# Kernel optimization log

Hardware: AMD Instinct MI355X
Metric: run time of the kernel (lower is better)

The kernel has to match this reference:

```python
import jax, jax.numpy as jnp
import numpy as np

D_MODEL = 1024
NHEAD = 16
HEAD_DIM = D_MODEL // NHEAD
SCALE = HEAD_DIM ** (-0.5)


def setup_inputs() -> dict:
    key = jax.random.key(0)
    k1, k2, k3 = jax.random.split(key, 3)
    B, T, C = 2, 2048, D_MODEL
    x = jax.random.normal(k1, (B, T, C), dtype=jnp.float32)
    W_qkv = jax.random.normal(k2, (3 * C, C), dtype=jnp.float32) * (C ** -0.5)
    b_qkv = jnp.zeros((3 * C,), dtype=jnp.float32)
    W_out = jax.random.normal(k3, (C, C), dtype=jnp.float32) * (C ** -0.5)
    b_out = jnp.zeros((C,), dtype=jnp.float32)
    return {"x": x, "W_qkv": W_qkv, "b_qkv": b_qkv, "W_out": W_out, "b_out": b_out}


def reference(x, W_qkv, b_qkv, W_out, b_out):
    B, T, C = x.shape
    H, hd = NHEAD, HEAD_DIM
    qkv = x @ W_qkv.T + b_qkv
    qkv = qkv.reshape(B, T, 3, H, hd).transpose(2, 0, 3, 1, 4)
    q, k, v = qkv[0], qkv[1], qkv[2]
    # scaled dot-product scores: (B,H,T,T)
    attn = jnp.einsum('bhqd,bhkd->bhqk', q, k) * SCALE
    # causal mask (is_causal=True): lower-triangular allowed
    causal = jnp.tril(jnp.ones((T, T), dtype=bool))
    attn = jnp.where(causal[None, None, :, :], attn, -jnp.inf)
    attn = jax.nn.softmax(attn, axis=-1)
    # (B,H,T,hd) -> (B,T,C)
    out = jnp.einsum('bhqk,bhkd->bhqd', attn, v)
    out = out.transpose(0, 2, 1, 3).reshape(B, T, C)
    out = out @ W_out.T + b_out
    return out
```

## Files before the change

kernel.cpp:

```cpp
#include <hip/hip_runtime.h>
#include <hip/hip_bf16.h>
#include <stdint.h>

#define D_MODEL 1024
#define NHEAD   16
#define HEAD_DIM 64
#define BATCH   2
#define SEQ     2048
#define M_TOK   (BATCH*SEQ)
#define N_QKV   (3*D_MODEL)
#define KDIM    1024
#define Q_SCALE (0.125f * 1.44269504088896f)

typedef __bf16 bf16_t;
typedef bf16_t bf16x8 __attribute__((ext_vector_type(8)));
typedef bf16_t bf16x4 __attribute__((ext_vector_type(4)));
typedef float  f32x4  __attribute__((ext_vector_type(4)));

__device__ __forceinline__ void gl_lds16(const void* g, void* l) {
    __builtin_amdgcn_global_load_lds(
        (__attribute__((address_space(1))) void*)(void*)(const_cast<void*>(g)),
        (__attribute__((address_space(3))) void*)l, 16, 0, 0);
}

#define N4_X  (M_TOK * KDIM / 4)
#define N4_W1 (N_QKV * KDIM / 4)
#define N4_W2 (D_MODEL * KDIM / 4)
__global__ void convert_all(const float* __restrict__ x,
                            const float* __restrict__ w1,
                            const float* __restrict__ w2,
                            bf16_t* __restrict__ ox,
                            bf16_t* __restrict__ o1,
                            bf16_t* __restrict__ o2) {
    int t = blockIdx.x * blockDim.x + threadIdx.x;
    const float* src;
    bf16_t* dst;
    int off;
    if (t < N4_X)                { src = x;  dst = ox; off = t; }
    else if (t < N4_X + N4_W1)   { src = w1; dst = o1; off = t - N4_X; }
    else                         { src = w2; dst = o2; off = t - N4_X - N4_W1; }
    float4 v = reinterpret_cast<const float4*>(src)[off];
    bf16x4 o = { (bf16_t)v.x, (bf16_t)v.y, (bf16_t)v.z, (bf16_t)v.w };
    reinterpret_cast<bf16x4*>(dst)[off] = o;
}

template <int MODE>
__global__ __launch_bounds__(256) void gemm_bt(
    const bf16_t* __restrict__ A,
    const bf16_t* __restrict__ Bw,
    const float*  __restrict__ bias,
    int N,
    bf16_t* __restrict__ qkv_out,
    bf16_t* __restrict__ vt_out,
    float*  __restrict__ f32_out)
{
    __shared__ bf16_t As[128 * 64];
    __shared__ bf16_t Bs[128 * 64];

    const int cpx = gridDim.x >> 3;
    const int bid = (blockIdx.x & 7) * cpx + (blockIdx.x >> 3);

    const int nbn = N / 128;
    const int bm = bid / nbn;
    const int bn = bid % nbn;
    const int m0 = bm * 128, n0 = bn * 128;
    const int tid = threadIdx.x, wave = tid >> 6, lane = tid & 63;
    const int wr = wave >> 1, wc = wave & 1;

    f32x4 acc[4][4] = {};

    const int srow = lane >> 3;
    const int scol = ((lane & 7) ^ srow) * 8;
    const bf16_t* gA0 = A  + (size_t)(m0 + wave * 32 + srow) * KDIM + scol;
    const bf16_t* gB0 = Bw + (size_t)(n0 + wave * 32 + srow) * KDIM + scol;
    bf16_t* lA0 = &As[(wave * 32) * 64];
    bf16_t* lB0 = &Bs[(wave * 32) * 64];

    const int fr = lane & 15;
    const int kq = lane >> 4;

    for (int k0 = 0; k0 < KDIM; k0 += 64) {
#pragma unroll
        for (int c = 0; c < 4; c++) {
            gl_lds16(gA0 + (size_t)(c * 8) * KDIM + k0, lA0 + (c * 8) * 64);
            gl_lds16(gB0 + (size_t)(c * 8) * KDIM + k0, lB0 + (c * 8) * 64);
        }
        __syncthreads();

        bf16x8 af[2][4], bfr[2][4];
#pragma unroll
        for (int kk = 0; kk < 2; kk++) {
            const int ch = (((kk << 2) | kq) ^ (fr & 7)) * 8;
#pragma unroll
            for (int i = 0; i < 4; i++)
                af[kk][i] = *reinterpret_cast<const bf16x8*>(
                    &As[(wr * 64 + i * 16 + fr) * 64 + ch]);
#pragma unroll
            for (int j = 0; j < 4; j++)
                bfr[kk][j] = *reinterpret_cast<const bf16x8*>(
                    &Bs[(wc * 64 + j * 16 + fr) * 64 + ch]);
        }
        __builtin_amdgcn_s_setprio(1);
#pragma unroll
        for (int i = 0; i < 4; i++)
#pragma unroll
            for (int j = 0; j < 4; j++) {
                acc[i][j] = __builtin_amdgcn_mfma_f32_16x16x32_bf16(
                    af[0][i], bfr[0][j], acc[i][j], 0, 0, 0);
                acc[i][j] = __builtin_amdgcn_mfma_f32_16x16x32_bf16(
                    af[1][i], bfr[1][j], acc[i][j], 0, 0, 0);
            }
        __builtin_amdgcn_s_setprio(0);
        __syncthreads();
    }

#pragma unroll
    for (int i = 0; i < 4; i++) {
#pragma unroll
        for (int j = 0; j < 4; j++) {
            const int col = n0 + wc * 64 + j * 16 + fr;
            const float bv = bias[col];
            const int row0 = m0 + wr * 64 + i * 16 + kq * 4;
            if (MODE == 1) {
#pragma unroll
                for (int r = 0; r < 4; r++)
                    f32_out[(size_t)(row0 + r) * N + col] = acc[i][j][r] + bv;
            } else if (col < 1024) {
#pragma unroll
                for (int r = 0; r < 4; r++)
                    qkv_out[(size_t)(row0 + r) * N_QKV + col] =
                        (bf16_t)((acc[i][j][r] + bv) * Q_SCALE);
            } else if (col < 2048) {
#pragma unroll
                for (int r = 0; r < 4; r++)
                    qkv_out[(size_t)(row0 + r) * N_QKV + col] =
                        (bf16_t)(acc[i][j][r] + bv);
            } else {
                const int d = col & 63, hh = (col >> 6) & 15;
                const int bb = row0 >> 11, t0 = row0 & 2047;
                bf16x4 pv = { (bf16_t)(acc[i][j][0] + bv),
                              (bf16_t)(acc[i][j][1] + bv),
                              (bf16_t)(acc[i][j][2] + bv),
                              (bf16_t)(acc[i][j][3] + bv) };
                *reinterpret_cast<bf16x4*>(
                    &vt_out[((size_t)((bb * NHEAD + hh) * HEAD_DIM + d)) * SEQ + t0]) = pv;
            }
        }
    }
}

__global__ __launch_bounds__(512) void attn_fwd(
    const bf16_t* __restrict__ qkv,
    const bf16_t* __restrict__ Vt,
    bf16_t* __restrict__ O)
{
    __shared__ bf16_t Ks[2][64 * 64];
    __shared__ bf16_t Vs[2][64 * 64];
    __shared__ bf16_t Ps[8][16 * 72];

    const int nqt = SEQ / 64;
    const int nbh = BATCH * NHEAD;
    const int qt = (nqt - 1) - (blockIdx.x / nbh);
    const int bh = blockIdx.x % nbh;
    const int b = bh >> 4, h = bh & 15;
    const int q0 = qt * 64;
    const int tid = threadIdx.x, wave = tid >> 6, lane = tid & 63;
    const int group = wave >> 2;
    const int w4 = wave & 3;
    const int fr = lane & 15;
    const int kq = lane >> 4;
    const int sw = fr & 7;
    const int c0 = (kq ^ sw) * 8;
    const int c1 = ((kq + 4) ^ sw) * 8;

    bf16x8 qf[2];
    {
        const size_t qrow = (size_t)(b * SEQ + q0 + w4 * 16 + fr);
        const int cbase = h * 64 + kq * 8;
        qf[0] = *reinterpret_cast<const bf16x8*>(&qkv[qrow * N_QKV + cbase]);
        qf[1] = *reinterpret_cast<const bf16x8*>(&qkv[qrow * N_QKV + cbase + 32]);
    }

    f32x4 acc_o[4] = {};
    float l_part = 0.f;

    const int srow = lane >> 3;
    const int scol = ((lane & 7) ^ srow) * 8;
    const bf16_t* gK = qkv + (size_t)(b * SEQ) * N_QKV + (D_MODEL + h * 64);
    const bf16_t* gV = Vt + (size_t)(bh * 64) * SEQ;

    const int nh0 = (qt + 2) >> 1;
    const int my_n = (group == 0) ? nh0 : (qt + 1 - nh0);
    const int base_t = (group == 0) ? 0 : nh0;

    for (int it = 0; it < nh0; ++it) {
        const bool act = (it < my_n);
        const int g_it = base_t + it;
        const int kv0 = g_it * 64;
        if (act) {
#pragma unroll
            for (int c = 0; c < 2; c++) {
                const int row = c * 32 + w4 * 8 + srow;
                gl_lds16(gK + (size_t)(kv0 + row) * N_QKV + scol,
                         &Ks[group][(c * 32 + w4 * 8) * 64]);
                gl_lds16(gV + (size_t)row * SEQ + kv0 + scol,
                         &Vs[group][(c * 32 + w4 * 8) * 64]);
            }
        }
        __syncthreads();

        if (act) {
            f32x4 s[4];
            __builtin_amdgcn_s_setprio(1);
#pragma unroll
            for (int j = 0; j < 4; j++) {
                bf16x8 k0f = *reinterpret_cast<const bf16x8*>(
                    &Ks[group][(j * 16 + fr) * 64 + c0]);
                bf16x8 k1f = *reinterpret_cast<const bf16x8*>(
                    &Ks[group][(j * 16 + fr) * 64 + c1]);
                f32x4 t = {0.f, 0.f, 0.f, 0.f};
                t = __builtin_amdgcn_mfma_f32_16x16x32_bf16(k0f, qf[0], t, 0, 0, 0);
                t = __builtin_amdgcn_mfma_f32_16x16x32_bf16(k1f, qf[1], t, 0, 0, 0);
                s[j] = t;
            }
            __builtin_amdgcn_s_setprio(0);

            if (g_it == qt) {
                const int qg = w4 * 16 + fr;
#pragma unroll
                for (int j = 0; j < 4; j++)
#pragma unroll
                    for (int r = 0; r < 4; r++)
                        if (j * 16 + kq * 4 + r > qg) s[j][r] = -1e30f;
            }

            float rs = 0.f;
#pragma unroll
            for (int j = 0; j < 4; j++)
#pragma unroll
                for (int r = 0; r < 4; r++) {
                    const float p = exp2f(s[j][r]);
                    s[j][r] = p;
                    rs += p;
                }
            l_part += rs;

#pragma unroll
            for (int j = 0; j < 4; j++) {
                bf16x4 pq = { (bf16_t)s[j][0], (bf16_t)s[j][1],
                              (bf16_t)s[j][2], (bf16_t)s[j][3] };
                *reinterpret_cast<bf16x4*>(&Ps[wave][fr * 72 + j * 16 + kq * 4]) = pq;
            }
            bf16x8 pb0 = *reinterpret_cast<const bf16x8*>(
                &Ps[wave][fr * 72 + kq * 8]);
            bf16x8 pb1 = *reinterpret_cast<const bf16x8*>(
                &Ps[wave][fr * 72 + 32 + kq * 8]);

            __builtin_amdgcn_s_setprio(1);
#pragma unroll
            for (int j = 0; j < 4; j++) {
                bf16x8 v0f = *reinterpret_cast<const bf16x8*>(
                    &Vs[group][(j * 16 + fr) * 64 + c0]);
                bf16x8 v1f = *reinterpret_cast<const bf16x8*>(
                    &Vs[group][(j * 16 + fr) * 64 + c1]);
                acc_o[j] = __builtin_amdgcn_mfma_f32_16x16x32_bf16(v0f, pb0, acc_o[j], 0, 0, 0);
                acc_o[j] = __builtin_amdgcn_mfma_f32_16x16x32_bf16(v1f, pb1, acc_o[j], 0, 0, 0);
            }
            __builtin_amdgcn_s_setprio(0);
        }

        __syncthreads();
    }

    float* Cf = reinterpret_cast<float*>(&Ps[0][0]);
    const int pbase = w4 * 1088;
    if (group == 1) {
#pragma unroll
        for (int j = 0; j < 4; j++)
#pragma unroll
            for (int r = 0; r < 4; r++)
                Cf[pbase + (j * 4 + r) * 64 + lane] = acc_o[j][r];
        Cf[pbase + 1024 + lane] = l_part;
    }
    __syncthreads();
    if (group == 0) {
#pragma unroll
        for (int j = 0; j < 4; j++)
#pragma unroll
            for (int r = 0; r < 4; r++)
                acc_o[j][r] += Cf[pbase + (j * 4 + r) * 64 + lane];
        l_part += Cf[pbase + 1024 + lane];

        l_part += __shfl_xor(l_part, 16);
        l_part += __shfl_xor(l_part, 32);
        const float inv = 1.0f / l_part;
        const size_t rowq = (size_t)(b * SEQ + q0 + w4 * 16 + fr);
#pragma unroll
        for (int j = 0; j < 4; j++) {
            bf16x4 ov = { (bf16_t)(acc_o[j][0] * inv), (bf16_t)(acc_o[j][1] * inv),
                          (bf16_t)(acc_o[j][2] * inv), (bf16_t)(acc_o[j][3] * inv) };
            *reinterpret_cast<bf16x4*>(&O[rowq * D_MODEL + h * 64 + j * 16 + kq * 4]) = ov;
        }
    }
}

extern "C" void kernel_launch(void* const* d_in, const int* in_sizes, int n_in,
                              void* d_out, int out_size, void* d_ws, size_t ws_size,
                              hipStream_t stream) {
    (void)in_sizes; (void)n_in; (void)out_size; (void)ws_size;
    const float* x    = (const float*)d_in[0];
    const float* Wqkv = (const float*)d_in[1];
    const float* bqkv = (const float*)d_in[2];
    const float* Wout = (const float*)d_in[3];
    const float* bout = (const float*)d_in[4];
    float* out = (float*)d_out;

    char* ws = (char*)d_ws;
    size_t off = 0;
    bf16_t* x_bf    = (bf16_t*)(ws + off); off += (size_t)M_TOK * KDIM * 2;
    bf16_t* wqkv_bf = (bf16_t*)(ws + off); off += (size_t)N_QKV * KDIM * 2;
    bf16_t* wout_bf = (bf16_t*)(ws + off); off += (size_t)D_MODEL * KDIM * 2;
    bf16_t* qkv     = (bf16_t*)(ws + off); off += (size_t)M_TOK * N_QKV * 2;
    bf16_t* vt      = (bf16_t*)(ws + off); off += (size_t)BATCH * NHEAD * HEAD_DIM * SEQ * 2;
    bf16_t* o_bf    = (bf16_t*)(ws + off); off += (size_t)M_TOK * D_MODEL * 2;

    convert_all<<<(N4_X + N4_W1 + N4_W2) / 256, 256, 0, stream>>>(
        x, Wqkv, Wout, x_bf, wqkv_bf, wout_bf);

    gemm_bt<0><<<(M_TOK / 128) * (N_QKV / 128), 256, 0, stream>>>(
        x_bf, wqkv_bf, bqkv, N_QKV, qkv, vt, nullptr);

    attn_fwd<<<BATCH * NHEAD * (SEQ / 64), 512, 0, stream>>>(qkv, vt, o_bf);

    gemm_bt<1><<<(M_TOK / 128) * (D_MODEL / 128), 256, 0, stream>>>(
        o_bf, wout_bf, bout, D_MODEL, nullptr, nullptr, out);
}
```

Before: 104.9 us.

## Double attention query tile to 128 rows per block, reusing K/V tiles

Each attention block now handles 128 query rows instead of 64, with each wave computing two 16-row query fragments against the same K/V LDS tiles. The KV range is split evenly between the two wave groups (qt2+1 tiles each), which removes the idle-iteration predicate. This halves K/V global loads per query and the number of blocks. In exchange it uses more registers and LDS, and launches half as many blocks (512), which may reduce occupancy and load balance across CUs.

Result: slower. 108.7 us (+3.6%).

```diff
diff --git a/kernel.cpp b/kernel.cpp
--- a/kernel.cpp
+++ b/kernel.cpp
@@ -156,14 +156,14 @@
 {
     __shared__ bf16_t Ks[2][64 * 64];
     __shared__ bf16_t Vs[2][64 * 64];
-    __shared__ bf16_t Ps[8][16 * 72];
-
-    const int nqt = SEQ / 64;
+    __shared__ bf16_t Ps[8][32 * 72];
+
+    const int nq2 = SEQ / 128;
     const int nbh = BATCH * NHEAD;
-    const int qt = (nqt - 1) - (blockIdx.x / nbh);
+    const int qt2 = (nq2 - 1) - (blockIdx.x / nbh);
     const int bh = blockIdx.x % nbh;
     const int b = bh >> 4, h = bh & 15;
-    const int q0 = qt * 64;
+    const int q0 = qt2 * 128;
     const int tid = threadIdx.x, wave = tid >> 6, lane = tid & 63;
     const int group = wave >> 2;
     const int w4 = wave & 3;
@@ -173,133 +173,164 @@
     const int c0 = (kq ^ sw) * 8;
     const int c1 = ((kq + 4) ^ sw) * 8;
 
-    bf16x8 qf[2];
+    bf16x8 qf0[2], qf1[2];
     {
-        const size_t qrow = (size_t)(b * SEQ + q0 + w4 * 16 + fr);
         const int cbase = h * 64 + kq * 8;
-        qf[0] = *reinterpret_cast<const bf16x8*>(&qkv[qrow * N_QKV + cbase]);
-        qf[1] = *reinterpret_cast<const bf16x8*>(&qkv[qrow * N_QKV + cbase + 32]);
-    }
-
-    f32x4 acc_o[4] = {};
-    float l_part = 0.f;
+        const size_t r0 = (size_t)(b * SEQ + q0 + w4 * 32 + fr);
+        const size_t r1 = r0 + 16;
+        qf0[0] = *reinterpret_cast<const bf16x8*>(&qkv[r0 * N_QKV + cbase]);
+        qf0[1] = *reinterpret_cast<const bf16x8*>(&qkv[r0 * N_QKV + cbase + 32]);
+        qf1[0] = *reinterpret_cast<const bf16x8*>(&qkv[r1 * N_QKV + cbase]);
+        qf1[1] = *reinterpret_cast<const bf16x8*>(&qkv[r1 * N_QKV + cbase + 32]);
+    }
+
+    f32x4 acc0[4] = {}, acc1[4] = {};
+    float l0 = 0.f, l1 = 0.f;
 
     const int srow = lane >> 3;
     const int scol = ((lane & 7) ^ srow) * 8;
     const bf16_t* gK = qkv + (size_t)(b * SEQ) * N_QKV + (D_MODEL + h * 64);
     const bf16_t* gV = Vt + (size_t)(bh * 64) * SEQ;
 
-    const int nh0 = (qt + 2) >> 1;
-    const int my_n = (group == 0) ? nh0 : (qt + 1 - nh0);
-    const int base_t = (group == 0) ? 0 : nh0;
-
-    for (int it = 0; it < nh0; ++it) {
-        const bool act = (it < my_n);
+    const int ntpg = qt2 + 1;
+    const int base_t = group * ntpg;
+
+    for (int it = 0; it < ntpg; ++it) {
         const int g_it = base_t + it;
         const int kv0 = g_it * 64;
-        if (act) {
-#pragma unroll
-            for (int c = 0; c < 2; c++) {
-                const int row = c * 32 + w4 * 8 + srow;
-                gl_lds16(gK + (size_t)(kv0 + row) * N_QKV + scol,
-                         &Ks[group][(c * 32 + w4 * 8) * 64]);
-                gl_lds16(gV + (size_t)row * SEQ + kv0 + scol,
-                         &Vs[group][(c * 32 + w4 * 8) * 64]);
-            }
+#pragma unroll
+        for (int c = 0; c < 2; c++) {
+            const int row = c * 32 + w4 * 8 + srow;
+            gl_lds16(gK + (size_t)(kv0 + row) * N_QKV + scol,
+                     &Ks[group][(c * 32 + w4 * 8) * 64]);
+            gl_lds16(gV + (size_t)row * SEQ + kv0 + scol,
+                     &Vs[group][(c * 32 + w4 * 8) * 64]);
         }
         __syncthreads();
 
-        if (act) {
-            f32x4 s[4];
-            __builtin_amdgcn_s_setprio(1);
-#pragma unroll
-            for (int j = 0; j < 4; j++) {
-                bf16x8 k0f = *reinterpret_cast<const bf16x8*>(
-                    &Ks[group][(j * 16 + fr) * 64 + c0]);
-                bf16x8 k1f = *reinterpret_cast<const bf16x8*>(
-                    &Ks[group][(j * 16 + fr) * 64 + c1]);
-                f32x4 t = {0.f, 0.f, 0.f, 0.f};
-                t = __builtin_amdgcn_mfma_f32_16x16x32_bf16(k0f, qf[0], t, 0, 0, 0);
-                t = __builtin_amdgcn_mfma_f32_16x16x32_bf16(k1f, qf[1], t, 0, 0, 0);
-                s[j] = t;
-            }
-            __builtin_amdgcn_s_setprio(0);
-
-            if (g_it == qt) {
-                const int qg = w4 * 16 + fr;
-#pragma unroll
-                for (int j = 0; j < 4; j++)
-#pragma unroll
-                    for (int r = 0; r < 4; r++)
-                        if (j * 16 + kq * 4 + r > qg) s[j][r] = -1e30f;
-            }
-
-            float rs = 0.f;
+        f32x4 s0[4], s1[4];
+        __builtin_amdgcn_s_setprio(1);
+#pragma unroll
+        for (int j = 0; j < 4; j++) {
+            bf16x8 k0f = *reinterpret_cast<const bf16x8*>(
+                &Ks[group][(j * 16 + fr) * 64 + c0]);
+            bf16x8 k1f = *reinterpret_cast<const bf16x8*>(
+                &Ks[group][(j * 16 + fr) * 64 + c1]);
+            f32x4 t = {0.f, 0.f, 0.f, 0.f};
+            t = __builtin_amdgcn_mfma_f32_16x16x32_bf16(k0f, qf0[0], t, 0, 0, 0);
+            t = __builtin_amdgcn_mfma_f32_16x16x32_bf16(k1f, qf0[1], t, 0, 0, 0);
+            s0[j] = t;
+            f32x4 u = {0.f, 0.f, 0.f, 0.f};
+            u = __builtin_amdgcn_mfma_f32_16x16x32_bf16(k0f, qf1[0], u, 0, 0, 0);
+            u = __builtin_amdgcn_mfma_f32_16x16x32_bf16(k1f, qf1[1], u, 0, 0, 0);
+            s1[j] = u;
+        }
+        __builtin_amdgcn_s_setprio(0);
+
+        if (g_it >= 2 * qt2) {
+            const int qg0 = q0 + w4 * 32 + fr;
+            const int qg1 = qg0 + 16;
 #pragma unroll
             for (int j = 0; j < 4; j++)
 #pragma unroll
                 for (int r = 0; r < 4; r++) {
-                    const float p = exp2f(s[j][r]);
-                    s[j][r] = p;
-                    rs += p;
+                    const int kvg = kv0 + j * 16 + kq * 4 + r;
+                    if (kvg > qg0) s0[j][r] = -1e30f;
+                    if (kvg > qg1) s1[j][r] = -1e30f;
                 }
-            l_part += rs;
-
-#pragma unroll
-            for (int j = 0; j < 4; j++) {
-                bf16x4 pq = { (bf16_t)s[j][0], (bf16_t)s[j][1],
-                              (bf16_t)s[j][2], (bf16_t)s[j][3] };
-                *reinterpret_cast<bf16x4*>(&Ps[wave][fr * 72 + j * 16 + kq * 4]) = pq;
-            }
-            bf16x8 pb0 = *reinterpret_cast<const bf16x8*>(
-                &Ps[wave][fr * 72 + kq * 8]);
-            bf16x8 pb1 = *reinterpret_cast<const bf16x8*>(
-                &Ps[wave][fr * 72 + 32 + kq * 8]);
-
-            __builtin_amdgcn_s_setprio(1);
-#pragma unroll
-            for (int j = 0; j < 4; j++) {
-                bf16x8 v0f = *reinterpret_cast<const bf16x8*>(
-                    &Vs[group][(j * 16 + fr) * 64 + c0]);
-                bf16x8 v1f = *reinterpret_cast<const bf16x8*>(
-                    &Vs[group][(j * 16 + fr) * 64 + c1]);
-                acc_o[j] = __builtin_amdgcn_mfma_f32_16x16x32_bf16(v0f, pb0, acc_o[j], 0, 0, 0);
-                acc_o[j] = __builtin_amdgcn_mfma_f32_16x16x32_bf16(v1f, pb1, acc_o[j], 0, 0, 0);
-            }
-            __builtin_amdgcn_s_setprio(0);
-        }
+        }
+
+        float rs0 = 0.f, rs1 = 0.f;
+#pragma unroll
+        for (int j = 0; j < 4; j++)
+#pragma unroll
+            for (int r = 0; r < 4; r++) {
+                const float p0 = exp2f(s0[j][r]);
+                const float p1 = exp2f(s1[j][r]);
+                s0[j][r] = p0;
+                s1[j][r] = p1;
+                rs0 += p0;
+                rs1 += p1;
+            }
+        l0 += rs0;
+        l1 += rs1;
+
+#pragma unroll
+        for (int j = 0; j < 4; j++) {
+            bf16x4 p0 = { (bf16_t)s0[j][0], (bf16_t)s0[j][1],
+                          (bf16_t)s0[j][2], (bf16_t)s0[j][3] };
+            *reinterpret_cast<bf16x4*>(&Ps[wave][fr * 72 + j * 16 + kq * 4]) = p0;
+            bf16x4 p1 = { (bf16_t)s1[j][0], (bf16_t)s1[j][1],
+                          (bf16_t)s1[j][2], (bf16_t)s1[j][3] };
+            *reinterpret_cast<bf16x4*>(&Ps[wave][(16 + fr) * 72 + j * 16 + kq * 4]) = p1;
+        }
+        bf16x8 pa0 = *reinterpret_cast<const bf16x8*>(
+            &Ps[wave][fr * 72 + kq * 8]);
+        bf16x8 pa1 = *reinterpret_cast<const bf16x8*>(
+            &Ps[wave][fr * 72 + 32 + kq * 8]);
+        bf16x8 pb0 = *reinterpret_cast<const bf16x8*>(
+            &Ps[wave][(16 + fr) * 72 + kq * 8]);
+        bf16x8 pb1 = *reinterpret_cast<const bf16x8*>(
+            &Ps[wave][(16 + fr) * 72 + 32 + kq * 8]);
+
+        __builtin_amdgcn_s_setprio(1);
+#pragma unroll
+        for (int j = 0; j < 4; j++) {
+            bf16x8 v0f = *reinterpret_cast<const bf16x8*>(
+                &Vs[group][(j * 16 + fr) * 64 + c0]);
+            bf16x8 v1f = *reinterpret_cast<const bf16x8*>(
+                &Vs[group][(j * 16 + fr) * 64 + c1]);
+            acc0[j] = __builtin_amdgcn_mfma_f32_16x16x32_bf16(v0f, pa0, acc0[j], 0, 0, 0);
+            acc0[j] = __builtin_amdgcn_mfma_f32_16x16x32_bf16(v1f, pa1, acc0[j], 0, 0, 0);
+            acc1[j] = __builtin_amdgcn_mfma_f32_16x16x32_bf16(v0f, pb0, acc1[j], 0, 0, 0);
+            acc1[j] = __builtin_amdgcn_mfma_f32_16x16x32_bf16(v1f, pb1, acc1[j], 0, 0, 0);
+        }
+        __builtin_amdgcn_s_setprio(0);
 
         __syncthreads();
     }
 
     float* Cf = reinterpret_cast<float*>(&Ps[0][0]);
-    const int pbase = w4 * 1088;
+    const int pbase = w4 * 2176;
     if (group == 1) {
 #pragma unroll
         for (int j = 0; j < 4; j++)
 #pragma unroll
-            for (int r = 0; r < 4; r++)
-                Cf[pbase + (j * 4 + r) * 64 + lane] = acc_o[j][r];
-        Cf[pbase + 1024 + lane] = l_part;
+            for (int r = 0; r < 4; r++) {
+                Cf[pbase + (j * 4 + r) * 64 + lane] = acc0[j][r];
+                Cf[pbase + 1088 + (j * 4 + r) * 64 + lane] = acc1[j][r];
+            }
+        Cf[pbase + 1024 + lane] = l0;
+        Cf[pbase + 1088 + 1024 + lane] = l1;
     }
     __syncthreads();
     if (group == 0) {
 #pragma unroll
         for (int j = 0; j < 4; j++)
 #pragma unroll
-            for (int r = 0; r < 4; r++)
-                acc_o[j][r] += Cf[pbase + (j * 4 + r) * 64 + lane];
-        l_part += Cf[pbase + 1024 + lane];
-
-        l_part += __shfl_xor(l_part, 16);
-        l_part += __shfl_xor(l_part, 32);
-        const float inv = 1.0f / l_part;
-        const size_t rowq = (size_t)(b * SEQ + q0 + w4 * 16 + fr);
-#pragma unroll
-        for (int j = 0; j < 4; j++) {
-            bf16x4 ov = { (bf16_t)(acc_o[j][0] * inv), (bf16_t)(acc_o[j][1] * inv),
-                          (bf16_t)(acc_o[j][2] * inv), (bf16_t)(acc_o[j][3] * inv) };
-            *reinterpret_cast<bf16x4*>(&O[rowq * D_MODEL + h * 64 + j * 16 + kq * 4]) = ov;
+            for (int r = 0; r < 4; r++) {
+                acc0[j][r] += Cf[pbase + (j * 4 + r) * 64 + lane];
+                acc1[j][r] += Cf[pbase + 1088 + (j * 4 + r) * 64 + lane];
+            }
+        l0 += Cf[pbase + 1024 + lane];
+        l1 += Cf[pbase + 1088 + 1024 + lane];
+
+        l0 += __shfl_xor(l0, 16);
+        l0 += __shfl_xor(l0, 32);
+        l1 += __shfl_xor(l1, 16);
+        l1 += __shfl_xor(l1, 32);
+        const float inv0 = 1.0f / l0;
+        const float inv1 = 1.0f / l1;
+        const size_t row0 = (size_t)(b * SEQ + q0 + w4 * 32 + fr);
+        const size_t row1 = row0 + 16;
+#pragma unroll
+        for (int j = 0; j < 4; j++) {
+            bf16x4 o0 = { (bf16_t)(acc0[j][0] * inv0), (bf16_t)(acc0[j][1] * inv0),
+                          (bf16_t)(acc0[j][2] * inv0), (bf16_t)(acc0[j][3] * inv0) };
+            *reinterpret_cast<bf16x4*>(&O[row0 * D_MODEL + h * 64 + j * 16 + kq * 4]) = o0;
+            bf16x4 o1 = { (bf16_t)(acc1[j][0] * inv1), (bf16_t)(acc1[j][1] * inv1),
+                          (bf16_t)(acc1[j][2] * inv1), (bf16_t)(acc1[j][3] * inv1) };
+            *reinterpret_cast<bf16x4*>(&O[row1 * D_MODEL + h * 64 + j * 16 + kq * 4]) = o1;
         }
     }
 }
@@ -330,7 +361,7 @@
     gemm_bt<0><<<(M_TOK / 128) * (N_QKV / 128), 256, 0, stream>>>(
         x_bf, wqkv_bf, bqkv, N_QKV, qkv, vt, nullptr);
 
-    attn_fwd<<<BATCH * NHEAD * (SEQ / 64), 512, 0, stream>>>(qkv, vt, o_bf);
+    attn_fwd<<<(SEQ / 128) * BATCH * NHEAD, 512, 0, stream>>>(qkv, vt, o_bf);
 
     gemm_bt<1><<<(M_TOK / 128) * (D_MODEL / 128), 256, 0, stream>>>(
         o_bf, wout_bf, bout, D_MODEL, nullptr, nullptr, out);
```
